# Kernel tuning notes

Measured on AMD Instinct MI355X. Metric: run time of the kernel, lower is better.

Reference implementation:

```python
import jax, jax.numpy as jnp
import numpy as np

D_IN = 2048
NUM_HEADS = 16
QK_NOPE = 64
QK_ROPE = 64
QK_HEAD = QK_NOPE + QK_ROPE  # 128
V_HEAD = 128
KV_LORA = 1024
SEQ = 4096
BATCH = 1
SCALE = QK_HEAD ** -0.5
EPS = 1e-6


def rmsnorm(x, w):
    return x * jax.lax.rsqrt(jnp.mean(x * x, axis=-1, keepdims=True) + EPS) * w


def apply_rope(x, cos, sin):
    # x: [B, S, H, D]; cos/sin: [S, D//2]; pairs are consecutive elements (view_as_complex)
    b, s, h, d = x.shape
    xr = x.reshape(b, s, h, d // 2, 2)
    xe, xo = xr[..., 0], xr[..., 1]
    c = cos[None, :, None, :]
    sn = sin[None, :, None, :]
    oe = xe * c - xo * sn
    oo = xe * sn + xo * c
    return jnp.stack([oe, oo], axis=-1).reshape(b, s, h, d)


def setup_inputs() -> dict:
    key = jax.random.key(0)
    ks = jax.random.split(key, 8)
    x = jax.random.normal(ks[0], (BATCH, SEQ, D_IN), dtype=jnp.float32)
    # rotary tables (rope_theta=10000)
    inv_freq = 1.0 / (10000.0 ** (np.arange(0, QK_ROPE, 2, dtype=np.float32) / QK_ROPE))
    angles = np.arange(SEQ, dtype=np.float32)[:, None] * inv_freq[None, :]
    cos = jnp.asarray(np.cos(angles), dtype=jnp.float32)
    sin = jnp.asarray(np.sin(angles), dtype=jnp.float32)
    # causal additive mask [S, S]
    mask = jnp.where(jnp.triu(jnp.ones((SEQ, SEQ), dtype=bool), k=1), -1e9, 0.0).astype(jnp.float32)
    def lin(k, fan_out, fan_in):
        bound = 1.0 / np.sqrt(fan_in)
        return jax.random.uniform(k, (fan_out, fan_in), jnp.float32, -bound, bound)
    wq = lin(ks[1], NUM_HEADS * QK_HEAD, D_IN)
    wkv_a = lin(ks[2], KV_LORA + QK_ROPE, D_IN)
    kv_norm_w = jnp.ones((KV_LORA,), dtype=jnp.float32)
    wkv_b = lin(ks[3], NUM_HEADS * (QK_NOPE + V_HEAD), KV_LORA)
    wo = lin(ks[4], D_IN, NUM_HEADS * V_HEAD)
    return {"x": x, "cos": cos, "sin": sin, "mask": mask, "wq": wq,
            "wkv_a": wkv_a, "kv_norm_w": kv_norm_w, "wkv_b": wkv_b, "wo": wo,
            "start_pos": 0}


def reference(x, cos, sin, mask, wq, wkv_a, kv_norm_w, wkv_b, wo, start_pos):
    b, s, _ = x.shape
    # Q projection -> [B, S, H, qk_head_dim]
    q = (x @ wq.T).reshape(b, s, NUM_HEADS, QK_HEAD)
    q_nope, q_pe = q[..., :QK_NOPE], q[..., QK_NOPE:]
    q_pe = apply_rope(q_pe, cos, sin)
    # KV low-rank projection
    kv_full = x @ wkv_a.T                               # [B, S, KV_LORA + QK_ROPE]
    kv, k_pe = kv_full[..., :KV_LORA], kv_full[..., KV_LORA:]
    k_pe = apply_rope(k_pe[:, :, None, :], cos, sin)    # [B, S, 1, QK_ROPE]
    # naive path: expand latent to per-head k_nope / v
    q = jnp.concatenate([q_nope, q_pe], axis=-1)        # [B, S, H, 128]
    kvb = (rmsnorm(kv, kv_norm_w) @ wkv_b.T).reshape(b, s, NUM_HEADS, QK_NOPE + V_HEAD)
    k_nope, v = kvb[..., :QK_NOPE], kvb[..., QK_NOPE:]
    k = jnp.concatenate([k_nope, jnp.broadcast_to(k_pe, (b, s, NUM_HEADS, QK_ROPE))], axis=-1)
    # start_pos=0 prefill: cache[:, :end_pos] == freshly written k, v
    scores = jnp.einsum('bqhd,bkhd->bqhk', q, k) * SCALE  # [B, S, H, S]
    scores = scores + mask[None, :, None, :]
    probs = jax.nn.softmax(scores.astype(jnp.float32), axis=-1).astype(x.dtype)
    out = jnp.einsum('bqhk,bkhd->bqhd', probs, v)       # [B, S, H, V_HEAD]
    return out.reshape(b, s, NUM_HEADS * V_HEAD) @ wo.T
```

## Files before the change

kernel.cpp:

```cpp
#include <hip/hip_runtime.h>

typedef __bf16 bf16;
typedef __attribute__((ext_vector_type(8))) __bf16 bf16x8;
typedef __attribute__((ext_vector_type(2))) __bf16 bf16x2;
typedef __attribute__((ext_vector_type(4))) float f32x4;
typedef __attribute__((ext_vector_type(4))) int int4v;

typedef __attribute__((address_space(1))) const void gconst_t;
typedef __attribute__((address_space(3))) void lvoid_t;

#define SEQ 4096
#define D_IN 2048
#define NHEADS 16
#define QSCALE (0.08838834764831843f * 1.4426950408889634f)
#define RMS_EPS 1e-6f
#define QKV_N 3136

__device__ inline unsigned pack2bf(float a, float b) {
    bf16x2 t; t[0] = (bf16)a; t[1] = (bf16)b;
    return __builtin_bit_cast(unsigned, t);
}

__device__ inline void conv_seg(const float* __restrict__ in, bf16* __restrict__ out,
                                int n, int i0, int stride) {
    for (int i = i0; i < n; i += stride) {
        float4 v = *reinterpret_cast<const float4*>(in + i);
        bf16 o[4];
        o[0] = (bf16)v.x; o[1] = (bf16)v.y; o[2] = (bf16)v.z; o[3] = (bf16)v.w;
        *reinterpret_cast<uint2*>(out + i) = *reinterpret_cast<uint2*>(o);
    }
}

__global__ __launch_bounds__(256) void convert_all_kernel(
    const float* __restrict__ xs,  const float* __restrict__ wqs,
    const float* __restrict__ was, const float* __restrict__ wbs,
    const float* __restrict__ wos,
    bf16* __restrict__ xd, bf16* __restrict__ wqd, bf16* __restrict__ wad,
    bf16* __restrict__ wbd, bf16* __restrict__ wod) {
    int i0 = (blockIdx.x * 256 + threadIdx.x) * 4;
    int stride = gridDim.x * 256 * 4;
    conv_seg(xs,  xd,  4096 * 2048, i0, stride);
    conv_seg(wqs, wqd, 2048 * 2048, i0, stride);
    conv_seg(was, wad, 1088 * 2048, i0, stride);
    conv_seg(wbs, wbd, 3072 * 1024, i0, stride);
    conv_seg(wos, wod, 2048 * 2048, i0, stride);
}

template<bool BF16_OUT>
__global__ __launch_bounds__(256) void gemm_bt_kernel(
    const bf16* __restrict__ A, const bf16* __restrict__ B, void* __restrict__ Cout,
    int M, int N, int K) {
    __shared__ __align__(16) bf16 Al[128 * 32];
    __shared__ __align__(16) bf16 Bl[128 * 32];
    int tid  = threadIdx.x;
    int lane = tid & 63;
    int w    = tid >> 6;
    int wr = w >> 1, wc = w & 1;
    int m0 = blockIdx.y * 128;
    int n0 = blockIdx.x * 128;
    int l15 = lane & 15;
    int g   = lane >> 4;

    int srow = (lane >> 2);
    int scol = (lane & 3) * 8;

    f32x4 acc[4][4] = {};

    for (int k0 = 0; k0 < K; k0 += 32) {
        __syncthreads();
        #pragma unroll
        for (int c = 0; c < 2; c++) {
            int arow = m0 + c*64 + w*16 + srow;
            const bf16* ga = A + (size_t)arow * K + k0 + scol;
            __builtin_amdgcn_global_load_lds((gconst_t*)ga, (lvoid_t*)&Al[c*2048 + w*512], 16, 0, 0);
            int brow = n0 + c*64 + w*16 + srow; if (brow >= N) brow = N - 1;
            const bf16* gb = B + (size_t)brow * K + k0 + scol;
            __builtin_amdgcn_global_load_lds((gconst_t*)gb, (lvoid_t*)&Bl[c*2048 + w*512], 16, 0, 0);
        }
        __syncthreads();
        bf16x8 af[4], bfv[4];
        #pragma unroll
        for (int mt = 0; mt < 4; mt++)
            af[mt] = *reinterpret_cast<const bf16x8*>(&Al[(wr*64 + mt*16 + l15) * 32 + g*8]);
        #pragma unroll
        for (int nt = 0; nt < 4; nt++)
            bfv[nt] = *reinterpret_cast<const bf16x8*>(&Bl[(wc*64 + nt*16 + l15) * 32 + g*8]);
        #pragma unroll
        for (int mt = 0; mt < 4; mt++)
            #pragma unroll
            for (int nt = 0; nt < 4; nt++)
                acc[mt][nt] = __builtin_amdgcn_mfma_f32_16x16x32_bf16(af[mt], bfv[nt], acc[mt][nt], 0, 0, 0);
    }

    #pragma unroll
    for (int mt = 0; mt < 4; mt++) {
        #pragma unroll
        for (int nt = 0; nt < 4; nt++) {
            int col = n0 + wc*64 + nt*16 + l15;
            if (col < N) {
                #pragma unroll
                for (int r = 0; r < 4; r++) {
                    int row = m0 + wr*64 + mt*16 + g*4 + r;
                    if (BF16_OUT)
                        ((bf16*)Cout)[(size_t)row * N + col] = (bf16)acc[mt][nt][r];
                    else
                        ((float*)Cout)[(size_t)row * N + col] = acc[mt][nt][r];
                }
            }
        }
    }
}

__global__ __launch_bounds__(256) void prep_q_kernel(
    bf16* __restrict__ qkv, const float* __restrict__ cosb, const float* __restrict__ sinb) {
    int s = blockIdx.x;
    int t = threadIdx.x;
    bf16* p = qkv + (size_t)s * QKV_N + t * 8;
    bf16x8 v = *reinterpret_cast<bf16x8*>(p);
    float f[8];
    #pragma unroll
    for (int j = 0; j < 8; j++) f[j] = (float)v[j];
    int d0 = (t & 15) * 8;
    if (d0 >= 64) {
        int ib = (d0 - 64) >> 1;
        #pragma unroll
        for (int pr = 0; pr < 4; pr++) {
            float c  = cosb[s * 32 + ib + pr];
            float sn = sinb[s * 32 + ib + pr];
            float xe = f[pr*2], xo = f[pr*2 + 1];
            f[pr*2]     = xe * c - xo * sn;
            f[pr*2 + 1] = xe * sn + xo * c;
        }
    }
    #pragma unroll
    for (int j = 0; j < 8; j++) v[j] = (bf16)(f[j] * QSCALE);
    *reinterpret_cast<bf16x8*>(p) = v;
}

__global__ __launch_bounds__(256) void prep_kv_kernel(
    const bf16* __restrict__ qkv, const float* __restrict__ w,
    const float* __restrict__ cosb, const float* __restrict__ sinb,
    bf16* __restrict__ kvnorm, bf16* __restrict__ kpe) {
    __shared__ float red[4];
    int s = blockIdx.x;
    int t = threadIdx.x;
    const bf16* src = qkv + (size_t)s * QKV_N + 2048;
    float f[4];
    {
        uint2 raw = *reinterpret_cast<const uint2*>(src + t * 4);
        bf16* vb = reinterpret_cast<bf16*>(&raw);
        float ss = 0.f;
        #pragma unroll
        for (int j = 0; j < 4; j++) { f[j] = (float)vb[j]; ss += f[j] * f[j]; }
        #pragma unroll
        for (int m = 1; m < 64; m <<= 1) ss += __shfl_xor(ss, m);
        if ((t & 63) == 0) red[t >> 6] = ss;
    }
    __syncthreads();
    float tot = red[0] + red[1] + red[2] + red[3];
    float rms = rsqrtf(tot * (1.0f / 1024.0f) + RMS_EPS);
    bf16 o[4];
    #pragma unroll
    for (int j = 0; j < 4; j++) o[j] = (bf16)(f[j] * rms * w[t*4 + j]);
    *reinterpret_cast<uint2*>(kvnorm + (size_t)s * 1024 + t * 4) = *reinterpret_cast<uint2*>(o);
    if (t < 16) {
        float e[4];
        #pragma unroll
        for (int j = 0; j < 4; j++) e[j] = (float)src[1024 + t*4 + j];
        int ib = t * 2;
        float c0 = cosb[s*32 + ib],     s0 = sinb[s*32 + ib];
        float c1 = cosb[s*32 + ib + 1], s1 = sinb[s*32 + ib + 1];
        bf16 ko[4];
        ko[0] = (bf16)(e[0]*c0 - e[1]*s0);
        ko[1] = (bf16)(e[0]*s0 + e[1]*c0);
        ko[2] = (bf16)(e[2]*c1 - e[3]*s1);
        ko[3] = (bf16)(e[2]*s1 + e[3]*c1);
        *reinterpret_cast<uint2*>(kpe + (size_t)s * 64 + t * 4) = *reinterpret_cast<uint2*>(ko);
    }
}

__global__ __launch_bounds__(256) void build_vt_kernel(
    const bf16* __restrict__ kvb, bf16* __restrict__ vt) {
    const int LT = 130;
    __shared__ bf16 lt[64 * 130];
    int h  = blockIdx.y;
    int s0 = blockIdx.x * 64;
    int t  = threadIdx.x;
    {
        int row = t >> 2;
        int d0  = (t & 3) * 32;
        const bf16* src = kvb + (size_t)(s0 + row) * 3072 + h * 192 + 64 + d0;
        int4v v0 = *reinterpret_cast<const int4v*>(src);
        int4v v1 = *reinterpret_cast<const int4v*>(src + 8);
        int4v v2 = *reinterpret_cast<const int4v*>(src + 16);
        int4v v3 = *reinterpret_cast<const int4v*>(src + 24);
        int* dst = reinterpret_cast<int*>(&lt[row * LT + d0]);
        int* s0p = reinterpret_cast<int*>(&v0); int* s1p = reinterpret_cast<int*>(&v1);
        int* s2p = reinterpret_cast<int*>(&v2); int* s3p = reinterpret_cast<int*>(&v3);
        #pragma unroll
        for (int j = 0; j < 4; j++) { dst[j] = s0p[j]; dst[4+j] = s1p[j]; dst[8+j] = s2p[j]; dst[12+j] = s3p[j]; }
    }
    __syncthreads();
    int ss = t & 63;
    int db = t >> 6;
    bf16* out = vt + (size_t)h * 128 * 4096 + s0 + ss;
    #pragma unroll
    for (int dd = db; dd < 128; dd += 4)
        out[(size_t)dd * 4096] = lt[ss * LT + dd];
}

__global__ __launch_bounds__(256, 2) void attn_kernel(
    const bf16* __restrict__ q,
    const bf16* __restrict__ kvb,
    const bf16* __restrict__ kpe,
    const bf16* __restrict__ vt,
    bf16* __restrict__ attn) {
    const int LPS = 72;
    __shared__ __align__(16) bf16 Kl[2][64 * 128];
    __shared__ __align__(16) bf16 Vl[2][128 * 64];
    __shared__ __align__(16) bf16 Pl[4][16 * 72];
    __shared__ __align__(16) float bcast[4][16];

    int h    = blockIdx.y;
    int tile = (h < 8) ? (31 - (int)blockIdx.x) : (int)blockIdx.x;
    int q0   = tile * 128;
    int t  = threadIdx.x;
    int lane = t & 63;
    int w  = t >> 6;
    int l15 = lane & 15;
    int g   = lane >> 4;
    int sw  = l15 & 7;
    int qrow = q0 + w * 32;

    const bf16* kvbh = kvb + h * 192;
    const bf16* vth  = vt + (size_t)h * 524288;

    bf16x8 qf[2][4];
    #pragma unroll
    for (int mt = 0; mt < 2; mt++) {
        const bf16* qp = q + (size_t)(qrow + mt*16 + l15) * QKV_N + h * 128 + g * 8;
        #pragma unroll
        for (int c = 0; c < 4; c++) qf[mt][c] = *reinterpret_cast<const bf16x8*>(qp + c * 32);
    }

    f32x4 o[2][8] = {};
    float mrow[2], lrow[2];
    #pragma unroll
    for (int mt = 0; mt < 2; mt++) { mrow[mt] = -3e38f; lrow[mt] = 0.f; }

    int nch = (q0 >> 6) + 2;
    int dc  = (q0 >> 6) + (w >> 1);

    auto stageK = [&](int jc, int buf) {
        int j0 = jc << 6;
        #pragma unroll
        for (int c = 0; c < 4; c++) {
            int idx = c*256 + w*64 + lane;
            int row = idx >> 4;
            int u   = (idx & 15) ^ (row & 7);
            const bf16* src = (u < 8)
                ? kvbh + (size_t)(j0 + row) * 3072 + u * 8
                : kpe  + (size_t)(j0 + row) * 64  + (u - 8) * 8;
            __builtin_amdgcn_global_load_lds((gconst_t*)src,
                (lvoid_t*)&Kl[buf][(c*256 + w*64) * 8], 16, 0, 0);
        }
    };
    auto stageV = [&](int jc, int buf) {
        int j0 = jc << 6;
        #pragma unroll
        for (int c = 0; c < 4; c++) {
            int idx = c*256 + w*64 + lane;
            int row = idx >> 3;
            int u   = (idx & 7) ^ (row & 7);
            const bf16* src = vth + (size_t)row * 4096 + j0 + u * 8;
            __builtin_amdgcn_global_load_lds((gconst_t*)src,
                (lvoid_t*)&Vl[buf][(c*256 + w*64) * 8], 16, 0, 0);
        }
    };

    stageK(0, 0); stageV(0, 0);

    for (int jc = 0; jc < nch; ++jc) {
        __syncthreads();
        if (jc + 1 < nch) { stageK(jc + 1, (jc + 1) & 1); stageV(jc + 1, (jc + 1) & 1); }

        if (jc <= dc) {
            int cur = jc & 1;
            int j0  = jc << 6;
            bool masked = (jc == dc);

            f32x4 sfr[2][4];
            __builtin_amdgcn_s_setprio(1);
            #pragma unroll
            for (int s = 0; s < 4; ++s) {
                int krow = s*16 + l15;
                bf16x8 kf[4];
                #pragma unroll
                for (int c = 0; c < 4; ++c)
                    kf[c] = *reinterpret_cast<const bf16x8*>(
                        &Kl[cur][krow*128 + (((c*4 + g) ^ sw) * 8)]);
                #pragma unroll
                for (int mt = 0; mt < 2; ++mt) {
                    f32x4 acc = {};
                    acc = __builtin_amdgcn_mfma_f32_16x16x32_bf16(kf[0], qf[mt][0], acc, 0, 0, 0);
                    acc = __builtin_amdgcn_mfma_f32_16x16x32_bf16(kf[1], qf[mt][1], acc, 0, 0, 0);
                    acc = __builtin_amdgcn_mfma_f32_16x16x32_bf16(kf[2], qf[mt][2], acc, 0, 0, 0);
                    acc = __builtin_amdgcn_mfma_f32_16x16x32_bf16(kf[3], qf[mt][3], acc, 0, 0, 0);
                    sfr[mt][s] = acc;
                }
            }
            __builtin_amdgcn_s_setprio(0);

            bf16x8 pf[2][2];
            #pragma unroll
            for (int mt = 0; mt < 2; ++mt) {
                int i = qrow + mt*16 + l15;
                if (masked) {
                    #pragma unroll
                    for (int s = 0; s < 4; ++s)
                        #pragma unroll
                        for (int r = 0; r < 4; ++r) {
                            int j = j0 + s*16 + g*4 + r;
                            if (j > i) sfr[mt][s][r] = -3e38f;
                        }
                }
                float m01 = fmaxf(fmaxf(sfr[mt][0][0], sfr[mt][0][1]),
                                  fmaxf(sfr[mt][0][2], sfr[mt][0][3]));
                float m23 = fmaxf(fmaxf(sfr[mt][1][0], sfr[mt][1][1]),
                                  fmaxf(sfr[mt][1][2], sfr[mt][1][3]));
                float m45 = fmaxf(fmaxf(sfr[mt][2][0], sfr[mt][2][1]),
                                  fmaxf(sfr[mt][2][2], sfr[mt][2][3]));
                float m67 = fmaxf(fmaxf(sfr[mt][3][0], sfr[mt][3][1]),
                                  fmaxf(sfr[mt][3][2], sfr[mt][3][3]));
                float mloc = fmaxf(fmaxf(m01, m23), fmaxf(m45, m67));
                float mx = fmaxf(mloc, __shfl_xor(mloc, 16));
                mx = fmaxf(mx, __shfl_xor(mx, 32));
                bool need = mx > mrow[mt];
                float mnew = fmaxf(mrow[mt], mx);
                float sfac = __builtin_amdgcn_exp2f(mrow[mt] - mnew);
                mrow[mt] = mnew;
                float psum = 0.f;
                #pragma unroll
                for (int s = 0; s < 4; ++s)
                    #pragma unroll
                    for (int r = 0; r < 4; ++r) {
                        float p = __builtin_amdgcn_exp2f(sfr[mt][s][r] - mnew);
                        sfr[mt][s][r] = p;
                        psum += p;
                    }
                lrow[mt] = lrow[mt] * sfac + psum;
                #pragma unroll
                for (int s = 0; s < 4; ++s) {
                    unsigned u0 = pack2bf(sfr[mt][s][0], sfr[mt][s][1]);
                    unsigned u1 = pack2bf(sfr[mt][s][2], sfr[mt][s][3]);
                    *reinterpret_cast<unsigned*>(&Pl[w][l15 * LPS + s*16 + g*4])     = u0;
                    *reinterpret_cast<unsigned*>(&Pl[w][l15 * LPS + s*16 + g*4 + 2]) = u1;
                }
                if (g == 0) bcast[w][l15] = sfac;
                f32x4 sf4 = *reinterpret_cast<const f32x4*>(&bcast[w][g*4]);
                if (__any(need)) {
                    #pragma unroll
                    for (int dt = 0; dt < 8; ++dt)
                        #pragma unroll
                        for (int r = 0; r < 4; ++r) o[mt][dt][r] *= sf4[r];
                }
                pf[mt][0] = *reinterpret_cast<const bf16x8*>(&Pl[w][l15 * LPS + g * 8]);
                pf[mt][1] = *reinterpret_cast<const bf16x8*>(&Pl[w][l15 * LPS + 32 + g * 8]);
            }

            __builtin_amdgcn_s_setprio(1);
            #pragma unroll
            for (int dt = 0; dt < 8; ++dt) {
                int vrow = dt*16 + l15;
                bf16x8 va = *reinterpret_cast<const bf16x8*>(
                    &Vl[cur][vrow*64 + ((g ^ sw) * 8)]);
                bf16x8 vb = *reinterpret_cast<const bf16x8*>(
                    &Vl[cur][vrow*64 + (((4 + g) ^ sw) * 8)]);
                o[0][dt] = __builtin_amdgcn_mfma_f32_16x16x32_bf16(pf[0][0], va, o[0][dt], 0, 0, 0);
                o[0][dt] = __builtin_amdgcn_mfma_f32_16x16x32_bf16(pf[0][1], vb, o[0][dt], 0, 0, 0);
                o[1][dt] = __builtin_amdgcn_mfma_f32_16x16x32_bf16(pf[1][0], va, o[1][dt], 0, 0, 0);
                o[1][dt] = __builtin_amdgcn_mfma_f32_16x16x32_bf16(pf[1][1], vb, o[1][dt], 0, 0, 0);
            }
            __builtin_amdgcn_s_setprio(0);
        }
    }

    #pragma unroll
    for (int mt = 0; mt < 2; ++mt) {
        float l = lrow[mt];
        l += __shfl_xor(l, 16);
        l += __shfl_xor(l, 32);
        float linv = __builtin_amdgcn_rcpf(l);
        if (g == 0) bcast[w][l15] = linv;
        f32x4 li4 = *reinterpret_cast<const f32x4*>(&bcast[w][g*4]);
        #pragma unroll
        for (int r = 0; r < 4; ++r) {
            int i = qrow + mt*16 + g*4 + r;
            #pragma unroll
            for (int dt = 0; dt < 8; ++dt)
                attn[(size_t)i * 2048 + h * 128 + dt*16 + l15] = (bf16)(o[mt][dt][r] * li4[r]);
        }
    }
}

extern "C" void kernel_launch(void* const* d_in, const int* in_sizes, int n_in,
                              void* d_out, int out_size, void* d_ws, size_t ws_size,
                              hipStream_t stream) {
    const float* x    = (const float*)d_in[0];
    const float* cosb = (const float*)d_in[1];
    const float* sinb = (const float*)d_in[2];
    const float* wq   = (const float*)d_in[4];
    const float* wkva = (const float*)d_in[5];
    const float* kvw  = (const float*)d_in[6];
    const float* wkvb = (const float*)d_in[7];
    const float* wo   = (const float*)d_in[8];

    char* ws = (char*)d_ws;
    bf16* x_bf    = (bf16*)(ws + 0);
    bf16* kvnorm  = (bf16*)(ws + 0);
    bf16* attn    = (bf16*)(ws + 0);
    bf16* wq_bf   = (bf16*)(ws + 16777216);
    bf16* wkva_bf = (bf16*)(ws + 25165824);
    bf16* wkvb_bf = (bf16*)(ws + 29622272);
    bf16* wo_bf   = (bf16*)(ws + 35913728);
    bf16* qkv     = (bf16*)(ws + 44302336);
    bf16* kpe     = (bf16*)(ws + 69992448);
    bf16* kvb     = (bf16*)(ws + 70516736);
    bf16* vt      = (bf16*)(ws + 95682560);

    convert_all_kernel<<<dim3(2048), dim3(256), 0, stream>>>(
        x, wq, wkva, wkvb, wo, x_bf, wq_bf, wkva_bf, wkvb_bf, wo_bf);

    gemm_bt_kernel<true><<<dim3(25, 32), dim3(256), 0, stream>>>(x_bf, wq_bf, qkv, 4096, QKV_N, 2048);

    prep_q_kernel <<<dim3(4096), dim3(256), 0, stream>>>(qkv, cosb, sinb);
    prep_kv_kernel<<<dim3(4096), dim3(256), 0, stream>>>(qkv, kvw, cosb, sinb, kvnorm, kpe);

    gemm_bt_kernel<true><<<dim3(24, 32), dim3(256), 0, stream>>>(kvnorm, wkvb_bf, kvb, 4096, 3072, 1024);

    build_vt_kernel<<<dim3(64, 16), dim3(256), 0, stream>>>(kvb, vt);

    attn_kernel<<<dim3(32, 16), dim3(256), 0, stream>>>(qkv, kvb, kpe, vt, attn);

    gemm_bt_kernel<false><<<dim3(16, 32), dim3(256), 0, stream>>>(attn, wo_bf, (float*)d_out, 4096, 2048, 2048);
}
```

Baseline: 373.5 us.

## Use 256-row double-buffered swizzled GEMM tiles and vmcnt-based pipelining in attention

Replaces the 128x128, K=32, single-buffered GEMM with a 512-thread kernel that computes 256xBN tiles over K=64 steps. It double-buffers and XOR-swizzles the LDS tiles and waits on outstanding loads with explicit vmcnt counters instead of full syncs. The goal is more data reuse per block, fewer barriers and overlap of global loads with MFMA work. The attention loop gets the same explicit vmcnt wait plus barrier scheme, so the next K/V chunk loads while the current one is computed. The larger tiles launch fewer blocks than there are CUs for some GEMMs, and the 128KB of LDS per block limits occupancy.

```diff
diff --git a/kernel.cpp b/kernel.cpp
--- a/kernel.cpp
+++ b/kernel.cpp
@@ -46,65 +46,107 @@
     conv_seg(wos, wod, 2048 * 2048, i0, stride);
 }
 
-template<bool BF16_OUT>
-__global__ __launch_bounds__(256) void gemm_bt_kernel(
+template<int BN, bool BF16_OUT>
+__global__ __launch_bounds__(512, 2) void gemm256_kernel(
     const bf16* __restrict__ A, const bf16* __restrict__ B, void* __restrict__ Cout,
     int M, int N, int K) {
-    __shared__ __align__(16) bf16 Al[128 * 32];
-    __shared__ __align__(16) bf16 Bl[128 * 32];
-    int tid  = threadIdx.x;
-    int lane = tid & 63;
-    int w    = tid >> 6;
-    int wr = w >> 1, wc = w & 1;
-    int m0 = blockIdx.y * 128;
-    int n0 = blockIdx.x * 128;
-    int l15 = lane & 15;
-    int g   = lane >> 4;
-
-    int srow = (lane >> 2);
-    int scol = (lane & 3) * 8;
-
-    f32x4 acc[4][4] = {};
-
-    for (int k0 = 0; k0 < K; k0 += 32) {
-        __syncthreads();
-        #pragma unroll
-        for (int c = 0; c < 2; c++) {
-            int arow = m0 + c*64 + w*16 + srow;
-            const bf16* ga = A + (size_t)arow * K + k0 + scol;
-            __builtin_amdgcn_global_load_lds((gconst_t*)ga, (lvoid_t*)&Al[c*2048 + w*512], 16, 0, 0);
-            int brow = n0 + c*64 + w*16 + srow; if (brow >= N) brow = N - 1;
-            const bf16* gb = B + (size_t)brow * K + k0 + scol;
-            __builtin_amdgcn_global_load_lds((gconst_t*)gb, (lvoid_t*)&Bl[c*2048 + w*512], 16, 0, 0);
-        }
-        __syncthreads();
-        bf16x8 af[4], bfv[4];
-        #pragma unroll
-        for (int mt = 0; mt < 4; mt++)
-            af[mt] = *reinterpret_cast<const bf16x8*>(&Al[(wr*64 + mt*16 + l15) * 32 + g*8]);
-        #pragma unroll
-        for (int nt = 0; nt < 4; nt++)
-            bfv[nt] = *reinterpret_cast<const bf16x8*>(&Bl[(wc*64 + nt*16 + l15) * 32 + g*8]);
-        #pragma unroll
-        for (int mt = 0; mt < 4; mt++)
-            #pragma unroll
-            for (int nt = 0; nt < 4; nt++)
-                acc[mt][nt] = __builtin_amdgcn_mfma_f32_16x16x32_bf16(af[mt], bfv[nt], acc[mt][nt], 0, 0, 0);
-    }
-
-    #pragma unroll
-    for (int mt = 0; mt < 4; mt++) {
-        #pragma unroll
-        for (int nt = 0; nt < 4; nt++) {
-            int col = n0 + wc*64 + nt*16 + l15;
+    constexpr int CB = BN / 64;
+    constexpr int NF = BN / 64;
+    constexpr int WC = BN / 4;
+    __shared__ __align__(16) bf16 Al[2][256 * 64];
+    __shared__ __align__(16) bf16 Bl[2][BN * 64];
+
+    int t    = threadIdx.x;
+    int lane = t & 63;
+    int w    = t >> 6;
+    int wr   = w >> 2;
+    int wc   = w & 3;
+    int l15  = lane & 15;
+    int g    = lane >> 4;
+    int m0 = blockIdx.y * 256;
+    int n0 = blockIdx.x * BN;
+
+    f32x4 acc[8][NF] = {};
+
+    auto stage = [&](int kt, int buf) {
+        int k0 = kt << 6;
+        #pragma unroll
+        for (int c = 0; c < 4; c++) {
+            int idx = c * 512 + t;
+            int r = idx >> 3;
+            int u = (idx & 7) ^ (r & 7);
+            const bf16* ga = A + (size_t)(m0 + r) * K + k0 + u * 8;
+            __builtin_amdgcn_global_load_lds((gconst_t*)ga,
+                (lvoid_t*)&Al[buf][(c * 512 + w * 64) * 8], 16, 0, 0);
+        }
+        #pragma unroll
+        for (int c = 0; c < CB; c++) {
+            int idx = c * 512 + t;
+            int r = idx >> 3;
+            int u = (idx & 7) ^ (r & 7);
+            int br = n0 + r; if (br >= N) br = N - 1;
+            const bf16* gb = B + (size_t)br * K + k0 + u * 8;
+            __builtin_amdgcn_global_load_lds((gconst_t*)gb,
+                (lvoid_t*)&Bl[buf][(c * 512 + w * 64) * 8], 16, 0, 0);
+        }
+    };
+
+    int nt = K >> 6;
+    stage(0, 0);
+    for (int kt = 0; kt < nt; ++kt) {
+        int buf = kt & 1;
+        if (kt + 1 < nt) {
+            stage(kt + 1, buf ^ 1);
+            __builtin_amdgcn_sched_barrier(0);
+            if constexpr (BN == 256) asm volatile("s_waitcnt vmcnt(8)" ::: "memory");
+            else                     asm volatile("s_waitcnt vmcnt(6)" ::: "memory");
+            __builtin_amdgcn_sched_barrier(0);
+        } else {
+            __builtin_amdgcn_sched_barrier(0);
+            asm volatile("s_waitcnt vmcnt(0)" ::: "memory");
+            __builtin_amdgcn_sched_barrier(0);
+        }
+        __builtin_amdgcn_s_barrier();
+
+        #pragma unroll
+        for (int ks = 0; ks < 2; ++ks) {
+            bf16x8 af[8], bfv[NF];
+            #pragma unroll
+            for (int mt = 0; mt < 8; mt++) {
+                int ra = wr * 128 + mt * 16 + l15;
+                int u = (ks * 4 + g) ^ (ra & 7);
+                af[mt] = *reinterpret_cast<const bf16x8*>(&Al[buf][ra * 64 + u * 8]);
+            }
+            #pragma unroll
+            for (int nf = 0; nf < NF; nf++) {
+                int rb = wc * WC + nf * 16 + l15;
+                int u = (ks * 4 + g) ^ (rb & 7);
+                bfv[nf] = *reinterpret_cast<const bf16x8*>(&Bl[buf][rb * 64 + u * 8]);
+            }
+            __builtin_amdgcn_s_setprio(1);
+            #pragma unroll
+            for (int mt = 0; mt < 8; mt++)
+                #pragma unroll
+                for (int nf = 0; nf < NF; nf++)
+                    acc[mt][nf] = __builtin_amdgcn_mfma_f32_16x16x32_bf16(af[mt], bfv[nf], acc[mt][nf], 0, 0, 0);
+            __builtin_amdgcn_s_setprio(0);
+        }
+        __builtin_amdgcn_s_barrier();
+    }
+
+    #pragma unroll
+    for (int mt = 0; mt < 8; mt++) {
+        #pragma unroll
+        for (int nf = 0; nf < NF; nf++) {
+            int col = n0 + wc * WC + nf * 16 + l15;
             if (col < N) {
                 #pragma unroll
                 for (int r = 0; r < 4; r++) {
-                    int row = m0 + wr*64 + mt*16 + g*4 + r;
+                    int row = m0 + wr * 128 + mt * 16 + g * 4 + r;
                     if (BF16_OUT)
-                        ((bf16*)Cout)[(size_t)row * N + col] = (bf16)acc[mt][nt][r];
+                        ((bf16*)Cout)[(size_t)row * N + col] = (bf16)acc[mt][nf][r];
                     else
-                        ((float*)Cout)[(size_t)row * N + col] = acc[mt][nt][r];
+                        ((float*)Cout)[(size_t)row * N + col] = acc[mt][nf][r];
                 }
             }
         }
@@ -242,6 +284,7 @@
         #pragma unroll
         for (int c = 0; c < 4; c++) qf[mt][c] = *reinterpret_cast<const bf16x8*>(qp + c * 32);
     }
+    asm volatile("s_waitcnt vmcnt(0)" ::: "memory");
 
     f32x4 o[2][8] = {};
     float mrow[2], lrow[2];
@@ -281,8 +324,17 @@
     stageK(0, 0); stageV(0, 0);
 
     for (int jc = 0; jc < nch; ++jc) {
-        __syncthreads();
-        if (jc + 1 < nch) { stageK(jc + 1, (jc + 1) & 1); stageV(jc + 1, (jc + 1) & 1); }
+        if (jc + 1 < nch) {
+            stageK(jc + 1, (jc + 1) & 1); stageV(jc + 1, (jc + 1) & 1);
+            __builtin_amdgcn_sched_barrier(0);
+            asm volatile("s_waitcnt vmcnt(8)" ::: "memory");
+            __builtin_amdgcn_sched_barrier(0);
+        } else {
+            __builtin_amdgcn_sched_barrier(0);
+            asm volatile("s_waitcnt vmcnt(0)" ::: "memory");
+            __builtin_amdgcn_sched_barrier(0);
+        }
+        __builtin_amdgcn_s_barrier();
 
         if (jc <= dc) {
             int cur = jc & 1;
@@ -383,6 +435,7 @@
             }
             __builtin_amdgcn_s_setprio(0);
         }
+        __builtin_amdgcn_s_barrier();
     }
 
     #pragma unroll
@@ -431,16 +484,16 @@
     convert_all_kernel<<<dim3(2048), dim3(256), 0, stream>>>(
         x, wq, wkva, wkvb, wo, x_bf, wq_bf, wkva_bf, wkvb_bf, wo_bf);
 
-    gemm_bt_kernel<true><<<dim3(25, 32), dim3(256), 0, stream>>>(x_bf, wq_bf, qkv, 4096, QKV_N, 2048);
+    gemm256_kernel<256, true><<<dim3(13, 16), dim3(512), 0, stream>>>(x_bf, wq_bf, qkv, 4096, QKV_N, 2048);
 
     prep_q_kernel <<<dim3(4096), dim3(256), 0, stream>>>(qkv, cosb, sinb);
     prep_kv_kernel<<<dim3(4096), dim3(256), 0, stream>>>(qkv, kvw, cosb, sinb, kvnorm, kpe);
 
-    gemm_bt_kernel<true><<<dim3(24, 32), dim3(256), 0, stream>>>(kvnorm, wkvb_bf, kvb, 4096, 3072, 1024);
+    gemm256_kernel<256, true><<<dim3(12, 16), dim3(512), 0, stream>>>(kvnorm, wkvb_bf, kvb, 4096, 3072, 1024);
 
     build_vt_kernel<<<dim3(64, 16), dim3(256), 0, stream>>>(kvb, vt);
 
     attn_kernel<<<dim3(32, 16), dim3(256), 0, stream>>>(qkv, kvb, kpe, vt, attn);
 
-    gemm_bt_kernel<false><<<dim3(16, 32), dim3(256), 0, stream>>>(attn, wo_bf, (float*)d_out, 4096, 2048, 2048);
-}
+    gemm256_kernel<128, false><<<dim3(16, 16), dim3(512), 0, stream>>>(attn, wo_bf, (float*)d_out, 4096, 2048, 2048);
+}
```

After: 336.5 us. 9.9% less time.
